# Kernel tuning notes

Hardware: AMD Instinct MI355X
Metric: run time of the kernel (lower is better)

The kernel has to match this reference:

```python
import jax, jax.numpy as jnp
import numpy as np

NUM_DIM = 1024
NUM_HEAD = 4


def setup_inputs() -> dict:
    key = jax.random.key(0)
    k1, k2, k3, k4, k5, k6 = jax.random.split(key, 6)
    B, N, C = 8, 2048, NUM_DIM
    x = jax.random.normal(k1, (B, N, C), dtype=jnp.float32)
    tmp_token = jax.random.normal(k2, (1, 1, C), dtype=jnp.float32)
    s = 1.0 / np.sqrt(C)
    Wqkv = jax.random.uniform(k3, (C, 3 * C), dtype=jnp.float32, minval=-s, maxval=s)
    bqkv = jax.random.uniform(k4, (3 * C,), dtype=jnp.float32, minval=-s, maxval=s)
    # Note: original module zero-inits v_proj; we use random weights for a
    # non-degenerate correctness baseline.
    Wv = jax.random.uniform(k5, (C, C), dtype=jnp.float32, minval=-s, maxval=s)
    bv = jax.random.uniform(k6, (C,), dtype=jnp.float32, minval=-s, maxval=s)
    return {"input": x, "tmp_token": tmp_token, "Wqkv": Wqkv, "bqkv": bqkv, "Wv": Wv, "bv": bv}


def reference(input, tmp_token, Wqkv, bqkv, Wv, bv):
    B = input.shape[0]
    # prepend learned token -> [B, N+1, C]
    x = jnp.concatenate([jnp.broadcast_to(tmp_token, (B, 1, tmp_token.shape[-1])), input], axis=1)
    B, N, C = x.shape
    H, Dh = NUM_HEAD, C // NUM_HEAD
    qkv = (x @ Wqkv + bqkv).reshape(B, N, 3, H, Dh)
    q = qkv[:, :, 0].transpose(0, 2, 1, 3)  # [B, H, N, Dh]
    k = qkv[:, :, 1].transpose(0, 2, 1, 3)
    v = qkv[:, :, 2].transpose(0, 2, 1, 3)
    scale = Dh ** (-0.5)
    scores = jnp.einsum("bhqd,bhkd->bhqk", q, k) * scale
    att = jax.nn.softmax(scores, axis=-1)  # dropout is identity in eval mode
    out = jnp.einsum("bhqk,bhkd->bhqd", att, v)
    out = out.transpose(0, 2, 1, 3).reshape(B, N, C)
    out = out @ Wv + bv  # op dropout identity in eval
    return out[:, 0, :]
```

## Files before the change

kernel.cpp:

```cpp
#include <hip/hip_runtime.h>
#include <math.h>

#define CDIM 1024
#define TC   3072
#define NIN  2048

#define OFF_Q0P 0
#define OFF_WS  16384
#define OFF_PS  20480
#define OFF_PY  24576
#define OFF_YB  4218880
#define OFF_OCP 4251648

__global__ void k_q0(const float* __restrict__ t, const float* __restrict__ W,
                     float* __restrict__ wsb) {
    int ic = blockIdx.x >> 3, jc = blockIdx.x & 7;
    int j = jc * 128 + threadIdx.x;
    int i0 = ic * 64;
    float acc = 0.f;
    for (int i = 0; i < 64; ++i)
        acc += t[i0 + i] * W[(size_t)(i0 + i) * TC + j];
    wsb[OFF_Q0P + ic * CDIM + j] = acc;
}

__global__ void k_ws(const float* __restrict__ W, const float* __restrict__ bqkv,
                     float* __restrict__ wsb) {
    int wave = threadIdx.x >> 6, lane = threadIdx.x & 63;
    int c = blockIdx.x, h = wave;
    int d0 = h * 256 + lane * 4;
    float4 wv = *(const float4*)&W[(size_t)c * TC + CDIM + d0];
    float4 q = *(const float4*)&bqkv[d0];
#pragma unroll
    for (int ic = 0; ic < 16; ++ic) {
        float4 p = *(const float4*)&wsb[OFF_Q0P + ic * CDIM + d0];
        q.x += p.x; q.y += p.y; q.z += p.z; q.w += p.w;
    }
    float acc = wv.x * q.x + wv.y * q.y + wv.z * q.z + wv.w * q.w;
    for (int off = 32; off > 0; off >>= 1) acc += __shfl_down(acc, off);
    if (lane == 0) wsb[OFF_WS + h * CDIM + c] = acc;
}

__global__ __launch_bounds__(256) void k_pass1(const float* __restrict__ x,
                                               float* __restrict__ wsb) {
    int tid = threadIdx.x, lane = tid & 63, wave = tid >> 6;
    int b = blockIdx.x >> 7, blkc = blockIdx.x & 127;

    float4 wsr[4][4];
#pragma unroll
    for (int k = 0; k < 4; ++k)
#pragma unroll
        for (int h = 0; h < 4; ++h)
            wsr[k][h] = *(const float4*)&wsb[OFF_WS + h * CDIM + k * 256 + lane * 4];

    float s[4] = {0.f, 0.f, 0.f, 0.f};
    float4 y[4][4];
#pragma unroll
    for (int h = 0; h < 4; ++h)
#pragma unroll
        for (int k = 0; k < 4; ++k) y[h][k] = make_float4(0.f, 0.f, 0.f, 0.f);

    const float* base = x + ((size_t)b * NIN + blkc * 16 + wave * 4) * CDIM;
#pragma unroll 2
    for (int i = 0; i < 4; ++i) {
        const float* row = base + (size_t)i * CDIM;
        float4 xv[4];
#pragma unroll
        for (int k = 0; k < 4; ++k) xv[k] = *(const float4*)&row[k * 256 + lane * 4];
        float e[4];
#pragma unroll
        for (int h = 0; h < 4; ++h) {
            float a = 0.f;
#pragma unroll
            for (int k = 0; k < 4; ++k)
                a += xv[k].x * wsr[k][h].x + xv[k].y * wsr[k][h].y +
                     xv[k].z * wsr[k][h].z + xv[k].w * wsr[k][h].w;
            for (int off = 1; off < 64; off <<= 1) a += __shfl_xor(a, off);
            e[h] = __expf(a * 0.0625f);
        }
#pragma unroll
        for (int h = 0; h < 4; ++h) {
            float f = e[h];
            s[h] += f;
#pragma unroll
            for (int k = 0; k < 4; ++k) {
                y[h][k].x += f * xv[k].x; y[h][k].y += f * xv[k].y;
                y[h][k].z += f * xv[k].z; y[h][k].w += f * xv[k].w;
            }
        }
    }

    __shared__ float ss[4][4];
    __shared__ float ybuf[4][CDIM];
    if (lane == 0)
#pragma unroll
        for (int h = 0; h < 4; ++h) ss[wave][h] = s[h];
    for (int idx = tid; idx < 4 * CDIM; idx += 256) ((float*)ybuf)[idx] = 0.f;
    __syncthreads();
    for (int w = 0; w < 4; ++w) {
        if (wave == w) {
#pragma unroll
            for (int h = 0; h < 4; ++h)
#pragma unroll
                for (int k = 0; k < 4; ++k) {
                    float4* dst = (float4*)&ybuf[h][k * 256 + lane * 4];
                    float4 v = *dst;
                    v.x += y[h][k].x; v.y += y[h][k].y;
                    v.z += y[h][k].z; v.w += y[h][k].w;
                    *dst = v;
                }
        }
        __syncthreads();
    }
    int p = blockIdx.x;
    if (tid < 4)
        wsb[OFF_PS + p * 4 + tid] = ss[0][tid] + ss[1][tid] + ss[2][tid] + ss[3][tid];
    for (int idx = tid; idx < 4 * CDIM; idx += 256)
        wsb[OFF_PY + (size_t)p * 4096 + idx] = ((float*)ybuf)[idx];
}

__global__ void k_comb(const float* __restrict__ t, float* __restrict__ wsb) {
    int tid = threadIdx.x, lane = tid & 63, wv = tid >> 6;
    int blk = blockIdx.x;
    int b = blk >> 4, h = (blk >> 2) & 3, cq = blk & 3;
    __shared__ float red[4], redS[4];

    int c0 = tid * 4;
    float4 tv = *(const float4*)&t[c0];
    float4 wsv = *(const float4*)&wsb[OFF_WS + h * CDIM + c0];
    float p = tv.x * wsv.x + tv.y * wsv.y + tv.z * wsv.z + tv.w * wsv.w;
    for (int off = 1; off < 64; off <<= 1) p += __shfl_xor(p, off);
    if (lane == 0) red[wv] = p;

    float sv = (tid < 128) ? wsb[OFF_PS + (size_t)(b * 128 + tid) * 4 + h] : 0.f;
    for (int off = 1; off < 64; off <<= 1) sv += __shfl_xor(sv, off);
    if (lane == 0) redS[wv] = sv;
    __syncthreads();
    float sc0 = (red[0] + red[1] + red[2] + red[3]) * 0.0625f;
    float e0 = __expf(sc0);
    float S = redS[0] + redS[1] + redS[2] + redS[3] + e0;

    int c = cq * 256 + tid;
    float acc = e0 * t[c];
#pragma unroll 4
    for (int j = 0; j < 128; ++j)
        acc += wsb[OFF_PY + (size_t)(b * 128 + j) * 4096 + h * CDIM + c];
    wsb[OFF_YB + (size_t)(b * 4 + h) * CDIM + c] = acc / S;
}

__global__ void k_ocy(const float* __restrict__ W, const float* __restrict__ bqkv,
                      float* __restrict__ wsb, float* __restrict__ out) {
    out[blockIdx.x * 128 + threadIdx.x] = 0.f;

    int p = blockIdx.x >> 3, q = blockIdx.x & 7;
    int h = p >> 1;
    __shared__ float sL[1024];
    for (int bb = 0; bb < 8; ++bb)
        sL[bb * 128 + threadIdx.x] = wsb[OFF_YB + (size_t)(bb * 4 + h) * CDIM + q * 128 + threadIdx.x];
    __syncthreads();
    int cp = p * 128 + threadIdx.x;
    float acc[8] = {0.f, 0.f, 0.f, 0.f, 0.f, 0.f, 0.f, 0.f};
    for (int c = 0; c < 128; ++c) {
        float wv = W[(size_t)(q * 128 + c) * TC + 2 * CDIM + cp];
#pragma unroll
        for (int bb = 0; bb < 8; ++bb) acc[bb] += sL[bb * 128 + c] * wv;
    }
    if (q == 0) {
        float bias = bqkv[2 * CDIM + cp];
#pragma unroll
        for (int bb = 0; bb < 8; ++bb) acc[bb] += bias;
    }
#pragma unroll
    for (int bb = 0; bb < 8; ++bb)
        wsb[OFF_OCP + (size_t)(q * 8 + bb) * CDIM + cp] = acc[bb];
}

__global__ void k_out(const float* __restrict__ Wv, const float* __restrict__ bv,
                      const float* __restrict__ wsb, float* __restrict__ out) {
    int jp = blockIdx.x >> 3, cq = blockIdx.x & 7;
    __shared__ float ocL[1024];
    for (int bb = 0; bb < 8; ++bb) {
        float sum = 0.f;
#pragma unroll
        for (int q = 0; q < 8; ++q)
            sum += wsb[OFF_OCP + (size_t)(q * 8 + bb) * CDIM + cq * 128 + threadIdx.x];
        ocL[bb * 128 + threadIdx.x] = sum;
    }
    __syncthreads();
    int j = jp * 128 + threadIdx.x;
    float acc[8] = {0.f, 0.f, 0.f, 0.f, 0.f, 0.f, 0.f, 0.f};
    for (int c = 0; c < 128; ++c) {
        float wv = Wv[(size_t)(cq * 128 + c) * CDIM + j];
#pragma unroll
        for (int bb = 0; bb < 8; ++bb) acc[bb] += ocL[bb * 128 + c] * wv;
    }
    if (cq == 0) {
        float bias = bv[j];
#pragma unroll
        for (int bb = 0; bb < 8; ++bb) acc[bb] += bias;
    }
#pragma unroll
    for (int bb = 0; bb < 8; ++bb) atomicAdd(&out[bb * CDIM + j], acc[bb]);
}

extern "C" void kernel_launch(void* const* d_in, const int* in_sizes, int n_in,
                              void* d_out, int out_size, void* d_ws, size_t ws_size,
                              hipStream_t stream) {
    const float* x    = (const float*)d_in[0];
    const float* t    = (const float*)d_in[1];
    const float* Wqkv = (const float*)d_in[2];
    const float* bqkv = (const float*)d_in[3];
    const float* Wv   = (const float*)d_in[4];
    const float* bv   = (const float*)d_in[5];
    float* wsb = (float*)d_ws;
    float* out = (float*)d_out;

    k_q0   <<<128,  128, 0, stream>>>(t, Wqkv, wsb);
    k_ws   <<<1024, 256, 0, stream>>>(Wqkv, bqkv, wsb);
    k_pass1<<<1024, 256, 0, stream>>>(x, wsb);
    k_comb <<<128,  256, 0, stream>>>(t, wsb);
    k_ocy  <<<64,   128, 0, stream>>>(Wqkv, bqkv, wsb, out);
    k_out  <<<64,   128, 0, stream>>>(Wv, bv, wsb, out);
}
```

Measured before the change: 179.2 us.

## Fuse all stages into one cooperative persistent kernel with grid syncs

Replaces six separate kernel launches with a single cooperative kernel of 256 blocks of 1024 threads, separated by grid-wide barriers. It also reshapes the pass-1 reduction so each block covers 64 rows, using shared-memory atomics, which shrinks the partial-sum buffers and the combine-stage work. The aim is to remove launch overhead and the inter-kernel gaps on a small problem. The cost is grid.sync latency and possibly lower occupancy during the streaming pass. It falls back to the old multi-kernel path if the cooperative launch fails.

New measurement: 498.7 us. 178% more time.

```diff
diff --git a/kernel.cpp b/kernel.cpp
--- a/kernel.cpp
+++ b/kernel.cpp
@@ -1,16 +1,215 @@
 #include <hip/hip_runtime.h>
+#include <hip/hip_cooperative_groups.h>
 #include <math.h>
+
+namespace cg = cooperative_groups;
 
 #define CDIM 1024
 #define TC   3072
 #define NIN  2048
 
+#define F_Q0P 0
+#define F_WS  16384
+#define F_PS  20480
+#define F_PY  21504
+#define F_YB  1070080
+#define F_OCP 1102848
+
+
+__global__ __launch_bounds__(1024, 4) void k_fused(
+    const float* __restrict__ x, const float* __restrict__ t,
+    const float* __restrict__ Wqkv, const float* __restrict__ bqkv,
+    const float* __restrict__ Wv, const float* __restrict__ bv,
+    float* __restrict__ wsb, float* __restrict__ out)
+{
+    cg::grid_group grid = cg::this_grid();
+    __shared__ float ybuf[4 * CDIM];
+    __shared__ float ps[4];
+    __shared__ float red[16];
+    int tid = threadIdx.x, lane = tid & 63, wave = tid >> 6;
+    int blk = blockIdx.x;
+
+    if (blk < 64) {
+        if (tid < 256) {
+            int ic = blk >> 2, jc = blk & 3;
+            int j = jc * 256 + tid;
+            int i0 = ic * 64;
+            float acc = 0.f;
+            for (int i = 0; i < 64; ++i)
+                acc += t[i0 + i] * Wqkv[(size_t)(i0 + i) * TC + j];
+            wsb[F_Q0P + ic * CDIM + j] = acc;
+        }
+    } else if (blk == 64) {
+        for (int r = 0; r < 8; ++r) out[r * 1024 + tid] = 0.f;
+    }
+    grid.sync();
+
+    if (tid < 256) {
+        float4 q = *(const float4*)&bqkv[tid * 4];
+#pragma unroll
+        for (int ic = 0; ic < 16; ++ic) {
+            float4 p = *(const float4*)&wsb[F_Q0P + ic * CDIM + tid * 4];
+            q.x += p.x; q.y += p.y; q.z += p.z; q.w += p.w;
+        }
+        *(float4*)&ybuf[tid * 4] = q;
+    }
+    __syncthreads();
+    {
+        int c = blk * 4 + (wave >> 2), h = wave & 3;
+        int d0 = h * 256 + lane * 4;
+        float4 wv = *(const float4*)&Wqkv[(size_t)c * TC + CDIM + d0];
+        float4 qv = *(const float4*)&ybuf[d0];
+        float a = wv.x * qv.x + wv.y * qv.y + wv.z * qv.z + wv.w * qv.w;
+        for (int off = 32; off > 0; off >>= 1) a += __shfl_down(a, off);
+        if (lane == 0) wsb[F_WS + h * CDIM + c] = a;
+    }
+    grid.sync();
+
+    {
+        float4 wsr[4][4];
+#pragma unroll
+        for (int k = 0; k < 4; ++k)
+#pragma unroll
+            for (int h = 0; h < 4; ++h)
+                wsr[k][h] = *(const float4*)&wsb[F_WS + h * CDIM + k * 256 + lane * 4];
+        float s[4] = {0.f, 0.f, 0.f, 0.f};
+        float4 y[4][4];
+#pragma unroll
+        for (int h = 0; h < 4; ++h)
+#pragma unroll
+            for (int k = 0; k < 4; ++k) y[h][k] = make_float4(0.f, 0.f, 0.f, 0.f);
+
+        int b = blk >> 5, ch = blk & 31;
+        const float* base = x + ((size_t)b * NIN + ch * 64 + wave * 4) * CDIM;
+#pragma unroll 2
+        for (int i = 0; i < 4; ++i) {
+            const float* row = base + (size_t)i * CDIM;
+            float4 xv[4];
+#pragma unroll
+            for (int k = 0; k < 4; ++k) xv[k] = *(const float4*)&row[k * 256 + lane * 4];
+            float e[4];
+#pragma unroll
+            for (int h = 0; h < 4; ++h) {
+                float a = 0.f;
+#pragma unroll
+                for (int k = 0; k < 4; ++k)
+                    a += xv[k].x * wsr[k][h].x + xv[k].y * wsr[k][h].y +
+                         xv[k].z * wsr[k][h].z + xv[k].w * wsr[k][h].w;
+                for (int off = 1; off < 64; off <<= 1) a += __shfl_xor(a, off);
+                e[h] = __expf(a * 0.0625f);
+            }
+#pragma unroll
+            for (int h = 0; h < 4; ++h) {
+                float f = e[h];
+                s[h] += f;
+#pragma unroll
+                for (int k = 0; k < 4; ++k) {
+                    y[h][k].x += f * xv[k].x; y[h][k].y += f * xv[k].y;
+                    y[h][k].z += f * xv[k].z; y[h][k].w += f * xv[k].w;
+                }
+            }
+        }
+        __syncthreads();
+        *(float4*)&ybuf[tid * 4] = make_float4(0.f, 0.f, 0.f, 0.f);
+        if (tid < 4) ps[tid] = 0.f;
+        __syncthreads();
+#pragma unroll
+        for (int h = 0; h < 4; ++h)
+#pragma unroll
+            for (int k = 0; k < 4; ++k) {
+                float* bp = &ybuf[h * 1024 + k * 256];
+                atomicAdd(&bp[0 * 64 + lane], y[h][k].x);
+                atomicAdd(&bp[1 * 64 + lane], y[h][k].y);
+                atomicAdd(&bp[2 * 64 + lane], y[h][k].z);
+                atomicAdd(&bp[3 * 64 + lane], y[h][k].w);
+            }
+        if (lane == 0)
+#pragma unroll
+            for (int h = 0; h < 4; ++h) atomicAdd(&ps[h], s[h]);
+        __syncthreads();
+        *(float4*)&wsb[F_PY + (size_t)blk * 4096 + tid * 4] = *(const float4*)&ybuf[tid * 4];
+        if (tid < 4) wsb[F_PS + blk * 4 + tid] = ps[tid];
+    }
+    grid.sync();
+
+    if (blk < 128) {
+        int b = blk >> 4, h = (blk >> 2) & 3, kq = blk & 3;
+        if (tid < 256) {
+            float4 tv = *(const float4*)&t[tid * 4];
+            float4 wsv = *(const float4*)&wsb[F_WS + h * CDIM + tid * 4];
+            float p = tv.x * wsv.x + tv.y * wsv.y + tv.z * wsv.z + tv.w * wsv.w;
+            for (int off = 1; off < 64; off <<= 1) p += __shfl_xor(p, off);
+            if (lane == 0) red[wave] = p;
+        }
+        if (wave == 0) {
+            float sv = (lane < 32) ? wsb[F_PS + (size_t)(b * 32 + lane) * 4 + h] : 0.f;
+            for (int off = 32; off > 0; off >>= 1) sv += __shfl_down(sv, off);
+            if (lane == 0) red[8] = sv;
+        }
+        __syncthreads();
+        float sc0 = (red[0] + red[1] + red[2] + red[3]) * 0.0625f;
+        float e0 = __expf(sc0);
+        float S = red[8] + e0;
+        if (tid < 256) {
+            int pidx = h * 1024 + kq * 256 + tid;
+            int c = kq * 256 + (tid & 63) * 4 + (tid >> 6);
+            float acc = 0.f;
+#pragma unroll 4
+            for (int m = 0; m < 32; ++m)
+                acc += wsb[F_PY + (size_t)(b * 32 + m) * 4096 + pidx];
+            wsb[F_YB + (size_t)(b * 4 + h) * CDIM + c] = (acc + e0 * t[c]) / S;
+        }
+    }
+    grid.sync();
+
+    if (blk < 128) {
+        int p = blk >> 4, q = blk & 15;
+        int h = p >> 1;
+        if (tid < 512) {
+            int bb = tid >> 6, cc = tid & 63;
+            ybuf[tid] = wsb[F_YB + (size_t)(bb * 4 + h) * CDIM + q * 64 + cc];
+        }
+        __syncthreads();
+        int bb = tid >> 7, cl = tid & 127;
+        int cp = p * 128 + cl;
+        float acc = 0.f;
+#pragma unroll 8
+        for (int c = 0; c < 64; ++c)
+            acc += ybuf[bb * 64 + c] * Wqkv[(size_t)(q * 64 + c) * TC + 2 * CDIM + cp];
+        if (q == 0) acc += bqkv[2 * CDIM + cp];
+        wsb[F_OCP + (size_t)(q * 8 + bb) * CDIM + cp] = acc;
+        __syncthreads();
+    }
+    grid.sync();
+
+    if (blk < 128) {
+        int jp = blk >> 4, cq = blk & 15;
+        if (tid < 512) {
+            int bb = tid >> 6, cc = tid & 63;
+            float sum = 0.f;
+#pragma unroll
+            for (int q = 0; q < 16; ++q)
+                sum += wsb[F_OCP + (size_t)(q * 8 + bb) * CDIM + cq * 64 + cc];
+            ybuf[tid] = sum;
+        }
+        __syncthreads();
+        int bb = tid >> 7, jl = tid & 127;
+        int j = jp * 128 + jl;
+        float acc = 0.f;
+#pragma unroll 8
+        for (int c = 0; c < 64; ++c)
+            acc += ybuf[bb * 64 + c] * Wv[(size_t)(cq * 64 + c) * CDIM + j];
+        if (cq == 0) acc += bv[j];
+        atomicAdd(&out[bb * CDIM + j], acc);
+    }
+}
+
 #define OFF_Q0P 0
 #define OFF_WS  16384
-#define OFF_PS  20480
-#define OFF_PY  24576
-#define OFF_YB  4218880
-#define OFF_OCP 4251648
+#define OFF_PS2 20480
+#define OFF_PY2 24576
+#define OFF_YB2 4218880
+#define OFF_OCP2 4251648
 
 __global__ void k_q0(const float* __restrict__ t, const float* __restrict__ W,
                      float* __restrict__ wsb) {
@@ -44,21 +243,18 @@
                                                float* __restrict__ wsb) {
     int tid = threadIdx.x, lane = tid & 63, wave = tid >> 6;
     int b = blockIdx.x >> 7, blkc = blockIdx.x & 127;
-
     float4 wsr[4][4];
 #pragma unroll
     for (int k = 0; k < 4; ++k)
 #pragma unroll
         for (int h = 0; h < 4; ++h)
             wsr[k][h] = *(const float4*)&wsb[OFF_WS + h * CDIM + k * 256 + lane * 4];
-
     float s[4] = {0.f, 0.f, 0.f, 0.f};
     float4 y[4][4];
 #pragma unroll
     for (int h = 0; h < 4; ++h)
 #pragma unroll
         for (int k = 0; k < 4; ++k) y[h][k] = make_float4(0.f, 0.f, 0.f, 0.f);
-
     const float* base = x + ((size_t)b * NIN + blkc * 16 + wave * 4) * CDIM;
 #pragma unroll 2
     for (int i = 0; i < 4; ++i) {
@@ -88,7 +284,6 @@
             }
         }
     }
-
     __shared__ float ss[4][4];
     __shared__ float ybuf[4][CDIM];
     if (lane == 0)
@@ -113,9 +308,9 @@
     }
     int p = blockIdx.x;
     if (tid < 4)
-        wsb[OFF_PS + p * 4 + tid] = ss[0][tid] + ss[1][tid] + ss[2][tid] + ss[3][tid];
+        wsb[OFF_PS2 + p * 4 + tid] = ss[0][tid] + ss[1][tid] + ss[2][tid] + ss[3][tid];
     for (int idx = tid; idx < 4 * CDIM; idx += 256)
-        wsb[OFF_PY + (size_t)p * 4096 + idx] = ((float*)ybuf)[idx];
+        wsb[OFF_PY2 + (size_t)p * 4096 + idx] = ((float*)ybuf)[idx];
 }
 
 __global__ void k_comb(const float* __restrict__ t, float* __restrict__ wsb) {
@@ -123,39 +318,35 @@
     int blk = blockIdx.x;
     int b = blk >> 4, h = (blk >> 2) & 3, cq = blk & 3;
     __shared__ float red[4], redS[4];
-
     int c0 = tid * 4;
     float4 tv = *(const float4*)&t[c0];
     float4 wsv = *(const float4*)&wsb[OFF_WS + h * CDIM + c0];
     float p = tv.x * wsv.x + tv.y * wsv.y + tv.z * wsv.z + tv.w * wsv.w;
     for (int off = 1; off < 64; off <<= 1) p += __shfl_xor(p, off);
     if (lane == 0) red[wv] = p;
-
-    float sv = (tid < 128) ? wsb[OFF_PS + (size_t)(b * 128 + tid) * 4 + h] : 0.f;
+    float sv = (tid < 128) ? wsb[OFF_PS2 + (size_t)(b * 128 + tid) * 4 + h] : 0.f;
     for (int off = 1; off < 64; off <<= 1) sv += __shfl_xor(sv, off);
     if (lane == 0) redS[wv] = sv;
     __syncthreads();
     float sc0 = (red[0] + red[1] + red[2] + red[3]) * 0.0625f;
     float e0 = __expf(sc0);
     float S = redS[0] + redS[1] + redS[2] + redS[3] + e0;
-
     int c = cq * 256 + tid;
     float acc = e0 * t[c];
 #pragma unroll 4
     for (int j = 0; j < 128; ++j)
-        acc += wsb[OFF_PY + (size_t)(b * 128 + j) * 4096 + h * CDIM + c];
-    wsb[OFF_YB + (size_t)(b * 4 + h) * CDIM + c] = acc / S;
+        acc += wsb[OFF_PY2 + (size_t)(b * 128 + j) * 4096 + h * CDIM + c];
+    wsb[OFF_YB2 + (size_t)(b * 4 + h) * CDIM + c] = acc / S;
 }
 
 __global__ void k_ocy(const float* __restrict__ W, const float* __restrict__ bqkv,
                       float* __restrict__ wsb, float* __restrict__ out) {
     out[blockIdx.x * 128 + threadIdx.x] = 0.f;
-
     int p = blockIdx.x >> 3, q = blockIdx.x & 7;
     int h = p >> 1;
     __shared__ float sL[1024];
     for (int bb = 0; bb < 8; ++bb)
-        sL[bb * 128 + threadIdx.x] = wsb[OFF_YB + (size_t)(bb * 4 + h) * CDIM + q * 128 + threadIdx.x];
+        sL[bb * 128 + threadIdx.x] = wsb[OFF_YB2 + (size_t)(bb * 4 + h) * CDIM + q * 128 + threadIdx.x];
     __syncthreads();
     int cp = p * 128 + threadIdx.x;
     float acc[8] = {0.f, 0.f, 0.f, 0.f, 0.f, 0.f, 0.f, 0.f};
@@ -171,7 +362,7 @@
     }
 #pragma unroll
     for (int bb = 0; bb < 8; ++bb)
-        wsb[OFF_OCP + (size_t)(q * 8 + bb) * CDIM + cp] = acc[bb];
+        wsb[OFF_OCP2 + (size_t)(q * 8 + bb) * CDIM + cp] = acc[bb];
 }
 
 __global__ void k_out(const float* __restrict__ Wv, const float* __restrict__ bv,
@@ -182,7 +373,7 @@
         float sum = 0.f;
 #pragma unroll
         for (int q = 0; q < 8; ++q)
-            sum += wsb[OFF_OCP + (size_t)(q * 8 + bb) * CDIM + cq * 128 + threadIdx.x];
+            sum += wsb[OFF_OCP2 + (size_t)(q * 8 + bb) * CDIM + cq * 128 + threadIdx.x];
         ocL[bb * 128 + threadIdx.x] = sum;
     }
     __syncthreads();
@@ -214,10 +405,16 @@
     float* wsb = (float*)d_ws;
     float* out = (float*)d_out;
 
-    k_q0   <<<128,  128, 0, stream>>>(t, Wqkv, wsb);
-    k_ws   <<<1024, 256, 0, stream>>>(Wqkv, bqkv, wsb);
-    k_pass1<<<1024, 256, 0, stream>>>(x, wsb);
-    k_comb <<<128,  256, 0, stream>>>(t, wsb);
-    k_ocy  <<<64,   128, 0, stream>>>(Wqkv, bqkv, wsb, out);
-    k_out  <<<64,   128, 0, stream>>>(Wv, bv, wsb, out);
-}
+    void* args[] = {(void*)&x, (void*)&t, (void*)&Wqkv, (void*)&bqkv,
+                    (void*)&Wv, (void*)&bv, (void*)&wsb, (void*)&out};
+    hipError_t err = hipLaunchCooperativeKernel((void*)k_fused, dim3(256), dim3(1024),
+                                                args, 0, stream);
+    if (err != hipSuccess) {
+        k_q0   <<<128,  128, 0, stream>>>(t, Wqkv, wsb);
+        k_ws   <<<1024, 256, 0, stream>>>(Wqkv, bqkv, wsb);
+        k_pass1<<<1024, 256, 0, stream>>>(x, wsb);
+        k_comb <<<128,  256, 0, stream>>>(t, wsb);
+        k_ocy  <<<64,   128, 0, stream>>>(Wqkv, bqkv, wsb, out);
+        k_out  <<<64,   128, 0, stream>>>(Wv, bv, wsb, out);
+    }
+}
```
